# Optimization experiments

Hardware: AMD Instinct MI355X
Metric: run time of the kernel (lower is better)

## Reference

```python
import jax, jax.numpy as jnp
import numpy as np

NUM_POINTS = 32
NUM_RESIDUALS = 2
DIST_THRESHOLD = 5.0
H = W = 128
C = 16


def setup_inputs() -> dict:
    key = jax.random.key(0)
    k = jax.random.split(key, 6)
    return {
        "md_maps": jax.random.uniform(k[0], (1, 3, H, W), dtype=jnp.float32),
        "dis_maps": jax.random.uniform(k[1], (1, 1, H, W), dtype=jnp.float32),
        "residual_maps": jax.random.uniform(k[2], (1, 1, H, W), dtype=jnp.float32),
        "features": jax.random.normal(k[3], (C, H, W), dtype=jnp.float32),
        "jloc": jax.random.uniform(k[4], (1, H, W), dtype=jnp.float32),
        "joff": jax.random.uniform(k[5], (2, H, W), dtype=jnp.float32),
        "topk": 300,
    }


def hafm_decoding(md_maps, dis_maps, residual_maps):
    scale = DIST_THRESHOLD
    b, _, h, w = md_maps.shape
    y0, x0 = jnp.meshgrid(jnp.arange(h, dtype=jnp.float32),
                          jnp.arange(w, dtype=jnp.float32), indexing='ij')
    y0 = y0[None, None]
    x0 = x0[None, None]
    sign_pad = jnp.arange(-NUM_RESIDUALS, NUM_RESIDUALS + 1, dtype=jnp.float32).reshape(1, -1, 1, 1)
    dist = jnp.clip(dis_maps + residual_maps * sign_pad, 0.0, 1.0)  # [B, 2R+1, H, W]
    md_un = (md_maps[:, :1] - 0.5) * np.pi * 2.0
    st_un = md_maps[:, 1:2] * np.pi / 2.0
    ed_un = -md_maps[:, 2:3] * np.pi / 2.0
    cs_md = jnp.cos(md_un)
    ss_md = jnp.sin(md_un)
    y_st = jnp.tan(st_un)
    y_ed = jnp.tan(ed_un)
    x_st_final = jnp.clip((cs_md - ss_md * y_st) * dist * scale + x0, 0.0, w - 1)
    y_st_final = jnp.clip((ss_md + cs_md * y_st) * dist * scale + y0, 0.0, h - 1)
    x_ed_final = jnp.clip((cs_md - ss_md * y_ed) * dist * scale + x0, 0.0, w - 1)
    y_ed_final = jnp.clip((ss_md + cs_md * y_ed) * dist * scale + y0, 0.0, h - 1)
    lines = jnp.stack((x_st_final, y_st_final, x_ed_final, y_ed_final), axis=-1)
    return lines.reshape(b, -1, 4)  # [B, (2R+1)*H*W, 4]


def compute_loi_features(features_per_image, lines_per_im, tspan):
    c, h, w = features_per_image.shape
    U, V = lines_per_im[:, :2], lines_per_im[:, 2:]
    pts = U[:, :, None] * tspan + V[:, :, None] * (1.0 - tspan) - 0.5  # [N, 2, P]
    pts = pts.transpose(0, 2, 1).reshape(-1, 2)  # [N*P, 2]
    px, py = pts[:, 0], pts[:, 1]
    px0 = jnp.clip(jnp.floor(px), 0.0, w - 1)
    py0 = jnp.clip(jnp.floor(py), 0.0, h - 1)
    px1 = jnp.clip(px0 + 1.0, 0.0, w - 1)
    py1 = jnp.clip(py0 + 1.0, 0.0, h - 1)
    px0l, py0l = px0.astype(jnp.int32), py0.astype(jnp.int32)
    px1l, py1l = px1.astype(jnp.int32), py1.astype(jnp.int32)
    xp = (features_per_image[:, py0l, px0l] * (py1 - py) * (px1 - px)
          + features_per_image[:, py1l, px0l] * (py - py0) * (px1 - px)
          + features_per_image[:, py0l, px1l] * (py1 - py) * (px - px0)
          + features_per_image[:, py1l, px1l] * (py - py0) * (px - px0))  # [C, N*P]
    xp = xp.reshape(c, -1, tspan.size).transpose(1, 0, 2)  # [N, C, P]
    return xp.reshape(xp.shape[0], -1)  # [N, C*P]


def non_maximum_suppression(a):
    # a: [B, 1, H, W]; torch max_pool2d pads with -inf for max pooling
    ap = jax.lax.reduce_window(a, -jnp.inf, jax.lax.max, (1, 1, 3, 3), (1, 1, 1, 1),
                               [(0, 0), (0, 0), (1, 1), (1, 1)])
    return a * (a == ap).astype(a.dtype)


def get_junctions(jloc, joff, topk):
    h, w = jloc.shape[-2], jloc.shape[-1]
    flat = jloc.reshape(-1)
    joff2 = joff.reshape(2, -1)
    scores, index = jax.lax.top_k(flat, topk)
    y = (index // w).astype(jnp.float32) + joff2[1][index] + 0.5
    x = (index % w).astype(jnp.float32) + joff2[0][index] + 0.5
    junctions = jnp.stack((x, y), axis=1)  # [topk, 2]
    return junctions, scores


def reference(md_maps, dis_maps, residual_maps, features, jloc, joff, topk):
    tspan = jnp.linspace(0.0, 1.0, NUM_POINTS, dtype=jnp.float32)[None, None, :]
    lines = hafm_decoding(md_maps, dis_maps, residual_maps)  # [1, 5*H*W, 4]
    loi = compute_loi_features(features, lines[0], tspan)    # [5*H*W, C*P]
    jloc_nms = non_maximum_suppression(jloc[None])            # [1, 1, H, W]
    junctions, scores = get_junctions(jloc_nms[0], joff, topk)
    return loi, junctions, scores
```

## Files before the change

### kernel.cpp

```cpp
#include <hip/hip_runtime.h>
#include <math.h>

#define HPX 128
#define WPX 128
#define HW  16384
#define CCH 16
#define NLINES 81920
#define NPTS 32
#define LOI_SIZE (NLINES * 512)
#define SORT_N 8192
#define NBINS 4096
#define CAND 1024

#define FEAT_T_OFF 0
#define LINES_OFF  1048576
#define KEYS_OFF   (1048576 + 1310720)
#define HIST_OFF   (KEYS_OFF + 65536)
#define CTR_OFF    (HIST_OFF + 16384)

__global__ __launch_bounds__(256) void transpose_feat(
        const float* __restrict__ feat, float* __restrict__ feat_t) {
    int tid = blockIdx.x * 256 + threadIdx.x;
    int pix = tid >> 4;
    int c   = tid & 15;
    feat_t[tid] = feat[c * HW + pix];
}

__global__ __launch_bounds__(256) void lines_kernel(
        const float* __restrict__ md,
        const float* __restrict__ dis,
        const float* __restrict__ res,
        float4* __restrict__ lines) {
    int line = blockIdx.x * 256 + threadIdx.x;
    int r    = line >> 14;
    int pix  = line & (HW - 1);
    int y0i  = pix >> 7, x0i = pix & 127;

    float md0 = md[pix], md1 = md[HW + pix], md2 = md[2 * HW + pix];
    float dv  = dis[pix], rv = res[pix];

    float dist = fminf(fmaxf(dv + rv * ((float)r - 2.0f), 0.0f), 1.0f);
    float d5   = dist * 5.0f;
    float md_un = (md0 - 0.5f) * 6.28318530717958647692f;
    float cs = cosf(md_un), ss = sinf(md_un);
    float y_st = tanf(md1 * 1.57079632679489661923f);
    float y_ed = tanf(-md2 * 1.57079632679489661923f);

    float x0f = (float)x0i, y0f = (float)y0i;
    float4 ep;
    ep.x = fminf(fmaxf((cs - ss * y_st) * d5 + x0f, 0.0f), 127.0f);
    ep.y = fminf(fmaxf((ss + cs * y_st) * d5 + y0f, 0.0f), 127.0f);
    ep.z = fminf(fmaxf((cs - ss * y_ed) * d5 + x0f, 0.0f), 127.0f);
    ep.w = fminf(fmaxf((ss + cs * y_ed) * d5 + y0f, 0.0f), 127.0f);
    lines[line] = ep;
}

__global__ __launch_bounds__(256) void nms_compact(
        const float* __restrict__ jloc,
        unsigned long long* __restrict__ keys,
        unsigned int* __restrict__ hist,
        unsigned int* __restrict__ ctr) {
    int pix = blockIdx.x * 256 + threadIdx.x;
    if (pix >= HW) return;
    int y = pix >> 7, x = pix & 127;
    float a = jloc[pix];
    float m = a;
    #pragma unroll
    for (int dy = -1; dy <= 1; dy++) {
        #pragma unroll
        for (int dx = -1; dx <= 1; dx++) {
            int yy = y + dy, xx = x + dx;
            if (yy >= 0 && yy < HPX && xx >= 0 && xx < WPX) {
                m = fmaxf(m, jloc[yy * WPX + xx]);
            }
        }
    }
    if (a == m && a > 0.0f) {
        unsigned int slot = atomicAdd(ctr, 1u);
        if (slot < SORT_N) {
            unsigned int bits = __float_as_uint(a);
            keys[slot] = ((unsigned long long)bits << 32)
                       | (unsigned long long)(0xFFFFFFFFu - (unsigned int)pix);
        }
        int bin = min(NBINS - 1, (int)(a * (float)NBINS));
        atomicAdd(&hist[bin], 1u);
    }
}

__global__ __launch_bounds__(1024) void select_topk(
        const unsigned long long* __restrict__ keys_g,
        const unsigned int* __restrict__ ctr,
        const unsigned int* __restrict__ hist,
        const float* __restrict__ joff,
        float* __restrict__ junc, float* __restrict__ scores, int topk) {
    __shared__ unsigned int h[NBINS];
    __shared__ unsigned long long cand[CAND];
    __shared__ unsigned int scount;
    __shared__ int Ts;
    int t = threadIdx.x;

    #pragma unroll
    for (int r = 0; r < 4; r++) h[t + r * 1024] = hist[t + r * 1024];
    if (t == 0) { scount = 0; Ts = 0; }
    __syncthreads();

    for (int off = 1; off < NBINS; off <<= 1) {
        unsigned int v[4];
        #pragma unroll
        for (int r = 0; r < 4; r++) {
            int i = t + r * 1024;
            v[r] = (i + off < NBINS) ? h[i + off] : 0u;
        }
        __syncthreads();
        #pragma unroll
        for (int r = 0; r < 4; r++) h[t + r * 1024] += v[r];
        __syncthreads();
    }

    #pragma unroll
    for (int r = 0; r < 4; r++) {
        int b = t + r * 1024;
        unsigned int sb = h[b];
        unsigned int sn = (b + 1 < NBINS) ? h[b + 1] : 0u;
        if (sb >= (unsigned int)topk && sn < (unsigned int)topk) Ts = b;
    }
    __syncthreads();
    int T = Ts;

    int n = min(ctr[0], (unsigned int)SORT_N);
    for (int i = t; i < n; i += 1024) {
        unsigned long long kk = keys_g[i];
        float val = __uint_as_float((unsigned int)(kk >> 32));
        int bin = min(NBINS - 1, (int)(val * (float)NBINS));
        if (bin >= T) {
            unsigned int p = atomicAdd(&scount, 1u);
            if (p < CAND) cand[p] = kk;
        }
    }
    __syncthreads();
    unsigned int sc = min(scount, (unsigned int)CAND);
    if (t >= (int)sc) cand[t] = 0ull;
    __syncthreads();

    for (int k = 2; k <= CAND; k <<= 1) {
        for (int j = k >> 1; j > 0; j >>= 1) {
            int ixj = t ^ j;
            if (ixj > t) {
                unsigned long long a = cand[t], b = cand[ixj];
                bool desc = ((t & k) == 0);
                if (desc ? (a < b) : (a > b)) { cand[t] = b; cand[ixj] = a; }
            }
            __syncthreads();
        }
    }

    if (t < topk) {
        unsigned long long kk = cand[t];
        float val = __uint_as_float((unsigned int)(kk >> 32));
        unsigned int idx = 0xFFFFFFFFu - (unsigned int)(kk & 0xFFFFFFFFull);
        if (idx >= HW) idx = 0;
        float xo = joff[idx];
        float yo = joff[HW + idx];
        junc[2 * t]     = (float)(idx & 127) + xo + 0.5f;
        junc[2 * t + 1] = (float)(idx >> 7)  + yo + 0.5f;
        scores[t] = val;
    }
}

__global__ __launch_bounds__(256) void loi_kernel(
        const float4* __restrict__ lines,
        const float* __restrict__ feat_t,
        float* __restrict__ out) {
    int tid  = blockIdx.x * 256 + threadIdx.x;
    int kq   = tid & 7;
    int line = tid >> 3;

    float4 ep = lines[line];
    float v[64];

    #pragma unroll
    for (int p = 0; p < 4; ++p) {
        int k = kq * 4 + p;
        float tk = (float)k * (1.0f / 31.0f);
        float px = ep.x * tk + ep.z * (1.0f - tk) - 0.5f;
        float py = ep.y * tk + ep.w * (1.0f - tk) - 0.5f;

        float px0 = fminf(fmaxf(floorf(px), 0.0f), 127.0f);
        float py0 = fminf(fmaxf(floorf(py), 0.0f), 127.0f);
        float px1 = fminf(px0 + 1.0f, 127.0f);
        float py1 = fminf(py0 + 1.0f, 127.0f);

        float wx1 = px - px0, wx0 = px1 - px;
        float wy1 = py - py0, wy0 = py1 - py;
        float w00 = wy0 * wx0, w01 = wy0 * wx1;
        float w10 = wy1 * wx0, w11 = wy1 * wx1;

        int b00 = (((int)py0) * WPX + (int)px0) * 4;
        int b01 = (((int)py0) * WPX + (int)px1) * 4;
        int b10 = (((int)py1) * WPX + (int)px0) * 4;
        int b11 = (((int)py1) * WPX + (int)px1) * 4;

        const float4* f4 = (const float4*)feat_t;
        #pragma unroll
        for (int cq = 0; cq < 4; ++cq) {
            float4 a = f4[b00 + cq], b = f4[b01 + cq];
            float4 c = f4[b10 + cq], d = f4[b11 + cq];
            v[(cq * 4 + 0) * 4 + p] = a.x * w00 + b.x * w01 + c.x * w10 + d.x * w11;
            v[(cq * 4 + 1) * 4 + p] = a.y * w00 + b.y * w01 + c.y * w10 + d.y * w11;
            v[(cq * 4 + 2) * 4 + p] = a.z * w00 + b.z * w01 + c.z * w10 + d.z * w11;
            v[(cq * 4 + 3) * 4 + p] = a.w * w00 + b.w * w01 + c.w * w10 + d.w * w11;
        }
    }

    float* ob = out + (size_t)line * 512 + kq * 4;
    #pragma unroll
    for (int c = 0; c < 16; ++c) {
        float4 st = make_float4(v[c * 4 + 0], v[c * 4 + 1], v[c * 4 + 2], v[c * 4 + 3]);
        *(float4*)(ob + c * 32) = st;
    }
}

extern "C" void kernel_launch(void* const* d_in, const int* in_sizes, int n_in,
                              void* d_out, int out_size, void* d_ws, size_t ws_size,
                              hipStream_t stream) {
    const float* md   = (const float*)d_in[0];
    const float* dis  = (const float*)d_in[1];
    const float* res  = (const float*)d_in[2];
    const float* feat = (const float*)d_in[3];
    const float* jloc = (const float*)d_in[4];
    const float* joff = (const float*)d_in[5];
    int topk = (out_size - LOI_SIZE) / 3;

    char* ws = (char*)d_ws;
    float* feat_t             = (float*)(ws + FEAT_T_OFF);
    float4* lines             = (float4*)(ws + LINES_OFF);
    unsigned long long* keys  = (unsigned long long*)(ws + KEYS_OFF);
    unsigned int* hist        = (unsigned int*)(ws + HIST_OFF);
    unsigned int* ctr         = (unsigned int*)(ws + CTR_OFF);

    float* out    = (float*)d_out;
    float* junc   = out + LOI_SIZE;
    float* scores = junc + 2 * topk;

    hipMemsetAsync(ws + HIST_OFF, 0, NBINS * 4 + 4, stream);

    transpose_feat<<<(HW * CCH) / 256, 256, 0, stream>>>(feat, feat_t);
    lines_kernel <<<NLINES / 256,      256, 0, stream>>>(md, dis, res, lines);
    nms_compact  <<<HW / 256,          256, 0, stream>>>(jloc, keys, hist, ctr);
    select_topk  <<<1,                1024, 0, stream>>>(keys, ctr, hist, joff, junc, scores, topk);
    loi_kernel   <<<(NLINES * 8) / 256, 256, 0, stream>>>(lines, feat_t, out);
}
```

Before: 228.9 us.

## Fuse prep kernels, replace histogram top-k with rank counting, nontemporal LOI stores

Merges the feature transpose, line decoding and NMS compaction into one block-partitioned launch, which cuts kernel launch overhead. The histogram-threshold plus bitonic-sort top-k is replaced by a single-block O(n^2) rank count over up to 4096 candidates held in shared memory. The large LOI output is written with nontemporal stores to reduce cache pollution. The rank-count loop serializes over n, so it may be slower when many NMS peaks exist, and candidates beyond 4096 are dropped.

```diff
diff --git a/kernel.cpp b/kernel.cpp
--- a/kernel.cpp
+++ b/kernel.cpp
@@ -8,162 +8,125 @@
 #define NLINES 81920
 #define NPTS 32
 #define LOI_SIZE (NLINES * 512)
-#define SORT_N 8192
-#define NBINS 4096
-#define CAND 1024
+#define SORT_N 4096
+
+typedef float vfloat4 __attribute__((ext_vector_type(4)));
 
 #define FEAT_T_OFF 0
 #define LINES_OFF  1048576
 #define KEYS_OFF   (1048576 + 1310720)
-#define HIST_OFF   (KEYS_OFF + 65536)
-#define CTR_OFF    (HIST_OFF + 16384)
-
-__global__ __launch_bounds__(256) void transpose_feat(
-        const float* __restrict__ feat, float* __restrict__ feat_t) {
-    int tid = blockIdx.x * 256 + threadIdx.x;
-    int pix = tid >> 4;
-    int c   = tid & 15;
-    feat_t[tid] = feat[c * HW + pix];
-}
-
-__global__ __launch_bounds__(256) void lines_kernel(
+#define CTR_OFF    (KEYS_OFF + 32768)
+
+#define TP_BLOCKS    1024
+#define LINE_BLOCKS  320
+#define NMS_BLOCKS   64
+#define PREP_BLOCKS  (TP_BLOCKS + LINE_BLOCKS + NMS_BLOCKS)
+
+__global__ __launch_bounds__(256) void prep_kernel(
+        const float* __restrict__ feat, float* __restrict__ feat_t,
         const float* __restrict__ md,
         const float* __restrict__ dis,
         const float* __restrict__ res,
-        float4* __restrict__ lines) {
-    int line = blockIdx.x * 256 + threadIdx.x;
-    int r    = line >> 14;
-    int pix  = line & (HW - 1);
-    int y0i  = pix >> 7, x0i = pix & 127;
-
-    float md0 = md[pix], md1 = md[HW + pix], md2 = md[2 * HW + pix];
-    float dv  = dis[pix], rv = res[pix];
-
-    float dist = fminf(fmaxf(dv + rv * ((float)r - 2.0f), 0.0f), 1.0f);
-    float d5   = dist * 5.0f;
-    float md_un = (md0 - 0.5f) * 6.28318530717958647692f;
-    float cs = cosf(md_un), ss = sinf(md_un);
-    float y_st = tanf(md1 * 1.57079632679489661923f);
-    float y_ed = tanf(-md2 * 1.57079632679489661923f);
-
-    float x0f = (float)x0i, y0f = (float)y0i;
-    float4 ep;
-    ep.x = fminf(fmaxf((cs - ss * y_st) * d5 + x0f, 0.0f), 127.0f);
-    ep.y = fminf(fmaxf((ss + cs * y_st) * d5 + y0f, 0.0f), 127.0f);
-    ep.z = fminf(fmaxf((cs - ss * y_ed) * d5 + x0f, 0.0f), 127.0f);
-    ep.w = fminf(fmaxf((ss + cs * y_ed) * d5 + y0f, 0.0f), 127.0f);
-    lines[line] = ep;
-}
-
-__global__ __launch_bounds__(256) void nms_compact(
+        float4* __restrict__ lines,
         const float* __restrict__ jloc,
         unsigned long long* __restrict__ keys,
-        unsigned int* __restrict__ hist,
         unsigned int* __restrict__ ctr) {
-    int pix = blockIdx.x * 256 + threadIdx.x;
-    if (pix >= HW) return;
-    int y = pix >> 7, x = pix & 127;
-    float a = jloc[pix];
-    float m = a;
-    #pragma unroll
-    for (int dy = -1; dy <= 1; dy++) {
+    int blk = blockIdx.x;
+    if (blk < TP_BLOCKS) {
+        int tid = blk * 256 + threadIdx.x;
+        int pix = tid >> 4;
+        int c   = tid & 15;
+        feat_t[tid] = feat[c * HW + pix];
+    } else if (blk < TP_BLOCKS + LINE_BLOCKS) {
+        int line = (blk - TP_BLOCKS) * 256 + threadIdx.x;
+        int r    = line >> 14;
+        int pix  = line & (HW - 1);
+        int y0i  = pix >> 7, x0i = pix & 127;
+
+        float md0 = md[pix], md1 = md[HW + pix], md2 = md[2 * HW + pix];
+        float dv  = dis[pix], rv = res[pix];
+
+        float dist = fminf(fmaxf(dv + rv * ((float)r - 2.0f), 0.0f), 1.0f);
+        float d5   = dist * 5.0f;
+        float md_un = (md0 - 0.5f) * 6.28318530717958647692f;
+        float cs = cosf(md_un), ss = sinf(md_un);
+        float y_st = tanf(md1 * 1.57079632679489661923f);
+        float y_ed = tanf(-md2 * 1.57079632679489661923f);
+
+        float x0f = (float)x0i, y0f = (float)y0i;
+        float4 ep;
+        ep.x = fminf(fmaxf((cs - ss * y_st) * d5 + x0f, 0.0f), 127.0f);
+        ep.y = fminf(fmaxf((ss + cs * y_st) * d5 + y0f, 0.0f), 127.0f);
+        ep.z = fminf(fmaxf((cs - ss * y_ed) * d5 + x0f, 0.0f), 127.0f);
+        ep.w = fminf(fmaxf((ss + cs * y_ed) * d5 + y0f, 0.0f), 127.0f);
+        lines[line] = ep;
+    } else {
+        int pix = (blk - TP_BLOCKS - LINE_BLOCKS) * 256 + threadIdx.x;
+        int y = pix >> 7, x = pix & 127;
+        float a = jloc[pix];
+        float m = a;
         #pragma unroll
-        for (int dx = -1; dx <= 1; dx++) {
-            int yy = y + dy, xx = x + dx;
-            if (yy >= 0 && yy < HPX && xx >= 0 && xx < WPX) {
-                m = fmaxf(m, jloc[yy * WPX + xx]);
+        for (int dy = -1; dy <= 1; dy++) {
+            #pragma unroll
+            for (int dx = -1; dx <= 1; dx++) {
+                int yy = y + dy, xx = x + dx;
+                if (yy >= 0 && yy < HPX && xx >= 0 && xx < WPX) {
+                    m = fmaxf(m, jloc[yy * WPX + xx]);
+                }
             }
         }
-    }
-    if (a == m && a > 0.0f) {
-        unsigned int slot = atomicAdd(ctr, 1u);
-        if (slot < SORT_N) {
-            unsigned int bits = __float_as_uint(a);
-            keys[slot] = ((unsigned long long)bits << 32)
-                       | (unsigned long long)(0xFFFFFFFFu - (unsigned int)pix);
-        }
-        int bin = min(NBINS - 1, (int)(a * (float)NBINS));
-        atomicAdd(&hist[bin], 1u);
+        if (a == m && a > 0.0f) {
+            unsigned int slot = atomicAdd(ctr, 1u);
+            if (slot < SORT_N) {
+                unsigned int bits = __float_as_uint(a);
+                keys[slot] = ((unsigned long long)bits << 32)
+                           | (unsigned long long)(0xFFFFFFFFu - (unsigned int)pix);
+            }
+        }
     }
 }
 
 __global__ __launch_bounds__(1024) void select_topk(
         const unsigned long long* __restrict__ keys_g,
         const unsigned int* __restrict__ ctr,
-        const unsigned int* __restrict__ hist,
         const float* __restrict__ joff,
         float* __restrict__ junc, float* __restrict__ scores, int topk) {
-    __shared__ unsigned int h[NBINS];
-    __shared__ unsigned long long cand[CAND];
-    __shared__ unsigned int scount;
-    __shared__ int Ts;
+    __shared__ unsigned long long sk[SORT_N];
     int t = threadIdx.x;
-
-    #pragma unroll
-    for (int r = 0; r < 4; r++) h[t + r * 1024] = hist[t + r * 1024];
-    if (t == 0) { scount = 0; Ts = 0; }
+    int n = (int)min(ctr[0], (unsigned int)SORT_N);
+
+    for (int i = t; i < n; i += 1024) sk[i] = keys_g[i];
     __syncthreads();
 
-    for (int off = 1; off < NBINS; off <<= 1) {
-        unsigned int v[4];
+    unsigned long long my[4];
+    int rank[4];
+    #pragma unroll
+    for (int q = 0; q < 4; q++) {
+        int i = t + q * 1024;
+        my[q] = (i < n) ? sk[i] : 0ull;
+        rank[q] = 0;
+    }
+
+    for (int j = 0; j < n; j++) {
+        unsigned long long kj = sk[j];
         #pragma unroll
-        for (int r = 0; r < 4; r++) {
-            int i = t + r * 1024;
-            v[r] = (i + off < NBINS) ? h[i + off] : 0u;
-        }
-        __syncthreads();
-        #pragma unroll
-        for (int r = 0; r < 4; r++) h[t + r * 1024] += v[r];
-        __syncthreads();
-    }
-
-    #pragma unroll
-    for (int r = 0; r < 4; r++) {
-        int b = t + r * 1024;
-        unsigned int sb = h[b];
-        unsigned int sn = (b + 1 < NBINS) ? h[b + 1] : 0u;
-        if (sb >= (unsigned int)topk && sn < (unsigned int)topk) Ts = b;
-    }
-    __syncthreads();
-    int T = Ts;
-
-    int n = min(ctr[0], (unsigned int)SORT_N);
-    for (int i = t; i < n; i += 1024) {
-        unsigned long long kk = keys_g[i];
-        float val = __uint_as_float((unsigned int)(kk >> 32));
-        int bin = min(NBINS - 1, (int)(val * (float)NBINS));
-        if (bin >= T) {
-            unsigned int p = atomicAdd(&scount, 1u);
-            if (p < CAND) cand[p] = kk;
-        }
-    }
-    __syncthreads();
-    unsigned int sc = min(scount, (unsigned int)CAND);
-    if (t >= (int)sc) cand[t] = 0ull;
-    __syncthreads();
-
-    for (int k = 2; k <= CAND; k <<= 1) {
-        for (int j = k >> 1; j > 0; j >>= 1) {
-            int ixj = t ^ j;
-            if (ixj > t) {
-                unsigned long long a = cand[t], b = cand[ixj];
-                bool desc = ((t & k) == 0);
-                if (desc ? (a < b) : (a > b)) { cand[t] = b; cand[ixj] = a; }
-            }
-            __syncthreads();
-        }
-    }
-
-    if (t < topk) {
-        unsigned long long kk = cand[t];
-        float val = __uint_as_float((unsigned int)(kk >> 32));
-        unsigned int idx = 0xFFFFFFFFu - (unsigned int)(kk & 0xFFFFFFFFull);
-        if (idx >= HW) idx = 0;
-        float xo = joff[idx];
-        float yo = joff[HW + idx];
-        junc[2 * t]     = (float)(idx & 127) + xo + 0.5f;
-        junc[2 * t + 1] = (float)(idx >> 7)  + yo + 0.5f;
-        scores[t] = val;
+        for (int q = 0; q < 4; q++) rank[q] += (kj > my[q]) ? 1 : 0;
+    }
+
+    #pragma unroll
+    for (int q = 0; q < 4; q++) {
+        int i = t + q * 1024;
+        if (i < n && rank[q] < topk) {
+            unsigned long long kk = my[q];
+            float val = __uint_as_float((unsigned int)(kk >> 32));
+            unsigned int idx = 0xFFFFFFFFu - (unsigned int)(kk & 0xFFFFFFFFull);
+            float xo = joff[idx];
+            float yo = joff[HW + idx];
+            int r = rank[q];
+            junc[2 * r]     = (float)(idx & 127) + xo + 0.5f;
+            junc[2 * r + 1] = (float)(idx >> 7)  + yo + 0.5f;
+            scores[r] = val;
+        }
     }
 }
 
@@ -215,8 +178,8 @@
     float* ob = out + (size_t)line * 512 + kq * 4;
     #pragma unroll
     for (int c = 0; c < 16; ++c) {
-        float4 st = make_float4(v[c * 4 + 0], v[c * 4 + 1], v[c * 4 + 2], v[c * 4 + 3]);
-        *(float4*)(ob + c * 32) = st;
+        vfloat4 st = { v[c * 4 + 0], v[c * 4 + 1], v[c * 4 + 2], v[c * 4 + 3] };
+        __builtin_nontemporal_store(st, (vfloat4*)(ob + c * 32));
     }
 }
 
@@ -235,18 +198,16 @@
     float* feat_t             = (float*)(ws + FEAT_T_OFF);
     float4* lines             = (float4*)(ws + LINES_OFF);
     unsigned long long* keys  = (unsigned long long*)(ws + KEYS_OFF);
-    unsigned int* hist        = (unsigned int*)(ws + HIST_OFF);
     unsigned int* ctr         = (unsigned int*)(ws + CTR_OFF);
 
     float* out    = (float*)d_out;
     float* junc   = out + LOI_SIZE;
     float* scores = junc + 2 * topk;
 
-    hipMemsetAsync(ws + HIST_OFF, 0, NBINS * 4 + 4, stream);
-
-    transpose_feat<<<(HW * CCH) / 256, 256, 0, stream>>>(feat, feat_t);
-    lines_kernel <<<NLINES / 256,      256, 0, stream>>>(md, dis, res, lines);
-    nms_compact  <<<HW / 256,          256, 0, stream>>>(jloc, keys, hist, ctr);
-    select_topk  <<<1,                1024, 0, stream>>>(keys, ctr, hist, joff, junc, scores, topk);
-    loi_kernel   <<<(NLINES * 8) / 256, 256, 0, stream>>>(lines, feat_t, out);
-}
+    (void)hipMemsetAsync(ctr, 0, 4, stream);
+
+    prep_kernel<<<PREP_BLOCKS, 256, 0, stream>>>(feat, feat_t, md, dis, res,
+                                                 lines, jloc, keys, ctr);
+    select_topk<<<1, 1024, 0, stream>>>(keys, ctr, joff, junc, scores, topk);
+    loi_kernel <<<(NLINES * 8) / 256, 256, 0, stream>>>(lines, feat_t, out);
+}
```

New measurement: 332.2 us. 1.45x slower.

## Fuse prep kernels, replace bitonic sort with rank selection, use nontemporal stores

Applied to the files above, without the earlier changes.

Merges the transpose, line decoding and NMS kernels into one launch whose blocks are split by role, which removes two launches. The bitonic sort in top-k selection is replaced by a counting rank computation, so each candidate scatters itself straight to its output slot. The large LOI output is written with nontemporal stores to keep it from polluting the cache. The key buffer is also halved, which risks dropping candidates if more than 4096 local maxima exist.

```diff
diff --git a/kernel.cpp b/kernel.cpp
--- a/kernel.cpp
+++ b/kernel.cpp
@@ -8,82 +8,87 @@
 #define NLINES 81920
 #define NPTS 32
 #define LOI_SIZE (NLINES * 512)
-#define SORT_N 8192
+#define SORT_N 4096
 #define NBINS 4096
 #define CAND 1024
+
+typedef float vfloat4 __attribute__((ext_vector_type(4)));
 
 #define FEAT_T_OFF 0
 #define LINES_OFF  1048576
 #define KEYS_OFF   (1048576 + 1310720)
-#define HIST_OFF   (KEYS_OFF + 65536)
+#define HIST_OFF   (KEYS_OFF + 32768)
 #define CTR_OFF    (HIST_OFF + 16384)
 
-__global__ __launch_bounds__(256) void transpose_feat(
-        const float* __restrict__ feat, float* __restrict__ feat_t) {
-    int tid = blockIdx.x * 256 + threadIdx.x;
-    int pix = tid >> 4;
-    int c   = tid & 15;
-    feat_t[tid] = feat[c * HW + pix];
-}
-
-__global__ __launch_bounds__(256) void lines_kernel(
+#define TP_BLOCKS    1024
+#define LINE_BLOCKS  320
+#define NMS_BLOCKS   64
+#define PREP_BLOCKS  (TP_BLOCKS + LINE_BLOCKS + NMS_BLOCKS)
+
+__global__ __launch_bounds__(256) void prep_kernel(
+        const float* __restrict__ feat, float* __restrict__ feat_t,
         const float* __restrict__ md,
         const float* __restrict__ dis,
         const float* __restrict__ res,
-        float4* __restrict__ lines) {
-    int line = blockIdx.x * 256 + threadIdx.x;
-    int r    = line >> 14;
-    int pix  = line & (HW - 1);
-    int y0i  = pix >> 7, x0i = pix & 127;
-
-    float md0 = md[pix], md1 = md[HW + pix], md2 = md[2 * HW + pix];
-    float dv  = dis[pix], rv = res[pix];
-
-    float dist = fminf(fmaxf(dv + rv * ((float)r - 2.0f), 0.0f), 1.0f);
-    float d5   = dist * 5.0f;
-    float md_un = (md0 - 0.5f) * 6.28318530717958647692f;
-    float cs = cosf(md_un), ss = sinf(md_un);
-    float y_st = tanf(md1 * 1.57079632679489661923f);
-    float y_ed = tanf(-md2 * 1.57079632679489661923f);
-
-    float x0f = (float)x0i, y0f = (float)y0i;
-    float4 ep;
-    ep.x = fminf(fmaxf((cs - ss * y_st) * d5 + x0f, 0.0f), 127.0f);
-    ep.y = fminf(fmaxf((ss + cs * y_st) * d5 + y0f, 0.0f), 127.0f);
-    ep.z = fminf(fmaxf((cs - ss * y_ed) * d5 + x0f, 0.0f), 127.0f);
-    ep.w = fminf(fmaxf((ss + cs * y_ed) * d5 + y0f, 0.0f), 127.0f);
-    lines[line] = ep;
-}
-
-__global__ __launch_bounds__(256) void nms_compact(
+        float4* __restrict__ lines,
         const float* __restrict__ jloc,
         unsigned long long* __restrict__ keys,
         unsigned int* __restrict__ hist,
         unsigned int* __restrict__ ctr) {
-    int pix = blockIdx.x * 256 + threadIdx.x;
-    if (pix >= HW) return;
-    int y = pix >> 7, x = pix & 127;
-    float a = jloc[pix];
-    float m = a;
-    #pragma unroll
-    for (int dy = -1; dy <= 1; dy++) {
-        #pragma unroll
-        for (int dx = -1; dx <= 1; dx++) {
-            int yy = y + dy, xx = x + dx;
-            if (yy >= 0 && yy < HPX && xx >= 0 && xx < WPX) {
-                m = fmaxf(m, jloc[yy * WPX + xx]);
+    int blk = blockIdx.x;
+    if (blk < TP_BLOCKS) {
+        int tid = blk * 256 + threadIdx.x;
+        int pix = tid >> 4;
+        int c   = tid & 15;
+        feat_t[tid] = feat[c * HW + pix];
+    } else if (blk < TP_BLOCKS + LINE_BLOCKS) {
+        int line = (blk - TP_BLOCKS) * 256 + threadIdx.x;
+        int r    = line >> 14;
+        int pix  = line & (HW - 1);
+        int y0i  = pix >> 7, x0i = pix & 127;
+
+        float md0 = md[pix], md1 = md[HW + pix], md2 = md[2 * HW + pix];
+        float dv  = dis[pix], rv = res[pix];
+
+        float dist = fminf(fmaxf(dv + rv * ((float)r - 2.0f), 0.0f), 1.0f);
+        float d5   = dist * 5.0f;
+        float md_un = (md0 - 0.5f) * 6.28318530717958647692f;
+        float cs = cosf(md_un), ss = sinf(md_un);
+        float y_st = tanf(md1 * 1.57079632679489661923f);
+        float y_ed = tanf(-md2 * 1.57079632679489661923f);
+
+        float x0f = (float)x0i, y0f = (float)y0i;
+        float4 ep;
+        ep.x = fminf(fmaxf((cs - ss * y_st) * d5 + x0f, 0.0f), 127.0f);
+        ep.y = fminf(fmaxf((ss + cs * y_st) * d5 + y0f, 0.0f), 127.0f);
+        ep.z = fminf(fmaxf((cs - ss * y_ed) * d5 + x0f, 0.0f), 127.0f);
+        ep.w = fminf(fmaxf((ss + cs * y_ed) * d5 + y0f, 0.0f), 127.0f);
+        lines[line] = ep;
+    } else {
+        int pix = (blk - TP_BLOCKS - LINE_BLOCKS) * 256 + threadIdx.x;
+        int y = pix >> 7, x = pix & 127;
+        float a = jloc[pix];
+        float m = a;
+        #pragma unroll
+        for (int dy = -1; dy <= 1; dy++) {
+            #pragma unroll
+            for (int dx = -1; dx <= 1; dx++) {
+                int yy = y + dy, xx = x + dx;
+                if (yy >= 0 && yy < HPX && xx >= 0 && xx < WPX) {
+                    m = fmaxf(m, jloc[yy * WPX + xx]);
+                }
             }
         }
-    }
-    if (a == m && a > 0.0f) {
-        unsigned int slot = atomicAdd(ctr, 1u);
-        if (slot < SORT_N) {
-            unsigned int bits = __float_as_uint(a);
-            keys[slot] = ((unsigned long long)bits << 32)
-                       | (unsigned long long)(0xFFFFFFFFu - (unsigned int)pix);
-        }
-        int bin = min(NBINS - 1, (int)(a * (float)NBINS));
-        atomicAdd(&hist[bin], 1u);
+        if (a == m && a > 0.0f) {
+            unsigned int slot = atomicAdd(ctr, 1u);
+            if (slot < SORT_N) {
+                unsigned int bits = __float_as_uint(a);
+                keys[slot] = ((unsigned long long)bits << 32)
+                           | (unsigned long long)(0xFFFFFFFFu - (unsigned int)pix);
+            }
+            int bin = min(NBINS - 1, (int)(a * (float)NBINS));
+            atomicAdd(&hist[bin], 1u);
+        }
     }
 }
 
@@ -94,7 +99,7 @@
         const float* __restrict__ joff,
         float* __restrict__ junc, float* __restrict__ scores, int topk) {
     __shared__ unsigned int h[NBINS];
-    __shared__ unsigned long long cand[CAND];
+    __shared__ unsigned long long cand[CAND + 8];
     __shared__ unsigned int scount;
     __shared__ int Ts;
     int t = threadIdx.x;
@@ -127,7 +132,7 @@
     __syncthreads();
     int T = Ts;
 
-    int n = min(ctr[0], (unsigned int)SORT_N);
+    int n = (int)min(ctr[0], (unsigned int)SORT_N);
     for (int i = t; i < n; i += 1024) {
         unsigned long long kk = keys_g[i];
         float val = __uint_as_float((unsigned int)(kk >> 32));
@@ -138,32 +143,29 @@
         }
     }
     __syncthreads();
-    unsigned int sc = min(scount, (unsigned int)CAND);
-    if (t >= (int)sc) cand[t] = 0ull;
-    __syncthreads();
-
-    for (int k = 2; k <= CAND; k <<= 1) {
-        for (int j = k >> 1; j > 0; j >>= 1) {
-            int ixj = t ^ j;
-            if (ixj > t) {
-                unsigned long long a = cand[t], b = cand[ixj];
-                bool desc = ((t & k) == 0);
-                if (desc ? (a < b) : (a > b)) { cand[t] = b; cand[ixj] = a; }
-            }
-            __syncthreads();
-        }
-    }
-
-    if (t < topk) {
-        unsigned long long kk = cand[t];
-        float val = __uint_as_float((unsigned int)(kk >> 32));
-        unsigned int idx = 0xFFFFFFFFu - (unsigned int)(kk & 0xFFFFFFFFull);
-        if (idx >= HW) idx = 0;
+    int sc = (int)min(scount, (unsigned int)CAND);
+    int padded = (sc + 7) & ~7;
+    if (t >= sc && t < padded + 8) cand[t] = 0ull;
+    __syncthreads();
+
+    unsigned long long my = (t < sc) ? cand[t] : 0ull;
+    int rank = 0;
+    for (int j = 0; j < padded; j += 8) {
+        unsigned long long kj[8];
+        #pragma unroll
+        for (int u = 0; u < 8; u++) kj[u] = cand[j + u];
+        #pragma unroll
+        for (int u = 0; u < 8; u++) rank += (kj[u] > my) ? 1 : 0;
+    }
+
+    if (t < sc && rank < topk) {
+        float val = __uint_as_float((unsigned int)(my >> 32));
+        unsigned int idx = 0xFFFFFFFFu - (unsigned int)(my & 0xFFFFFFFFull);
         float xo = joff[idx];
         float yo = joff[HW + idx];
-        junc[2 * t]     = (float)(idx & 127) + xo + 0.5f;
-        junc[2 * t + 1] = (float)(idx >> 7)  + yo + 0.5f;
-        scores[t] = val;
+        junc[2 * rank]     = (float)(idx & 127) + xo + 0.5f;
+        junc[2 * rank + 1] = (float)(idx >> 7)  + yo + 0.5f;
+        scores[rank] = val;
     }
 }
 
@@ -215,8 +217,8 @@
     float* ob = out + (size_t)line * 512 + kq * 4;
     #pragma unroll
     for (int c = 0; c < 16; ++c) {
-        float4 st = make_float4(v[c * 4 + 0], v[c * 4 + 1], v[c * 4 + 2], v[c * 4 + 3]);
-        *(float4*)(ob + c * 32) = st;
+        vfloat4 st = { v[c * 4 + 0], v[c * 4 + 1], v[c * 4 + 2], v[c * 4 + 3] };
+        __builtin_nontemporal_store(st, (vfloat4*)(ob + c * 32));
     }
 }
 
@@ -242,11 +244,10 @@
     float* junc   = out + LOI_SIZE;
     float* scores = junc + 2 * topk;
 
-    hipMemsetAsync(ws + HIST_OFF, 0, NBINS * 4 + 4, stream);
-
-    transpose_feat<<<(HW * CCH) / 256, 256, 0, stream>>>(feat, feat_t);
-    lines_kernel <<<NLINES / 256,      256, 0, stream>>>(md, dis, res, lines);
-    nms_compact  <<<HW / 256,          256, 0, stream>>>(jloc, keys, hist, ctr);
-    select_topk  <<<1,                1024, 0, stream>>>(keys, ctr, hist, joff, junc, scores, topk);
-    loi_kernel   <<<(NLINES * 8) / 256, 256, 0, stream>>>(lines, feat_t, out);
-}
+    (void)hipMemsetAsync(ws + HIST_OFF, 0, NBINS * 4 + 4, stream);
+
+    prep_kernel<<<PREP_BLOCKS, 256, 0, stream>>>(feat, feat_t, md, dis, res,
+                                                 lines, jloc, keys, hist, ctr);
+    select_topk<<<1, 1024, 0, stream>>>(keys, ctr, hist, joff, junc, scores, topk);
+    loi_kernel <<<(NLINES * 8) / 256, 256, 0, stream>>>(lines, feat_t, out);
+}
```

New measurement: 230.3 us. No clear change (+0.6%).
